# Optimization experiments

Measured on AMD Instinct MI355X. Metric: run time of the kernel, lower is better.

Reference implementation:

```python
import jax, jax.numpy as jnp
import numpy as np

B, IN, H = 262144, 128, 128

def setup_inputs() -> dict:
    key = jax.random.key(0)
    ks = jax.random.split(key, 16)
    s = 1.0 / np.sqrt(IN)
    inp = {
        'x': jax.random.normal(ks[0], (B, IN), jnp.float32),
        'h_prev': jax.random.normal(ks[1], (B, H), jnp.float32),
        'c_prev': jax.random.normal(ks[2], (B, H), jnp.float32),
        'n_prev': jax.random.uniform(ks[3], (B, H), jnp.float32),
        'W_i': jax.random.normal(ks[4], (H, IN), jnp.float32) * s,
        'U_i': jax.random.normal(ks[5], (H, H), jnp.float32) * s,
        'W_f': jax.random.normal(ks[6], (H, IN), jnp.float32) * s,
        'U_f': jax.random.normal(ks[7], (H, H), jnp.float32) * s,
        'W_o': jax.random.normal(ks[8], (H, IN), jnp.float32) * s,
        'U_o': jax.random.normal(ks[9], (H, H), jnp.float32) * s,
        'W_z': jax.random.normal(ks[10], (H, IN), jnp.float32) * s,
        'U_z': jax.random.normal(ks[11], (H, H), jnp.float32) * s,
        'b_i': jnp.zeros((H,), jnp.float32),
        'b_f': jnp.ones((H,), jnp.float32),
        'b_o': jnp.zeros((H,), jnp.float32),
        'b_z': jnp.zeros((H,), jnp.float32),
    }
    return inp

def reference(x, h_prev, c_prev, n_prev, W_i, U_i, W_f, U_f, W_o, U_o, W_z, U_z, b_i, b_f, b_o, b_z):
    # torch Linear(no bias): y = x @ W.T
    i_tilde = x @ W_i.T + h_prev @ U_i.T + b_i
    f_tilde = x @ W_f.T + h_prev @ U_f.T + b_f
    o_tilde = x @ W_o.T + h_prev @ U_o.T + b_o
    z_tilde = x @ W_z.T + h_prev @ U_z.T + b_z
    m_t = jnp.maximum(f_tilde, i_tilde)
    i_t = jnp.exp(i_tilde - m_t)
    f_t = jax.nn.sigmoid(f_tilde) + jnp.exp(f_tilde - m_t)
    o_t = jax.nn.sigmoid(o_tilde)
    z_t = jnp.tanh(z_tilde)
    c_t = f_t * c_prev + i_t * z_t
    n_t = f_t * n_prev + i_t
    h_t = o_t * (c_t / (n_t + 1e-8))
    return (h_t, c_t, n_t)
```

## Files before the change

### kernel.cpp

```cpp
#include <hip/hip_runtime.h>
#include <hip/hip_bf16.h>

typedef __attribute__((ext_vector_type(8))) _Float16 f16x8;
typedef __attribute__((ext_vector_type(4))) float f32x4;

#define NROWS 262144
#define MBLK  32
#define NBLKS (NROWS / MBLK)

__global__ void prep_weights(
    const float* __restrict__ Wi, const float* __restrict__ Ui,
    const float* __restrict__ Wf, const float* __restrict__ Uf,
    const float* __restrict__ Wo, const float* __restrict__ Uo,
    const float* __restrict__ Wz, const float* __restrict__ Uz,
    ushort* __restrict__ wh)
{
    int idx = blockIdx.x * 256 + threadIdx.x;
    int j    = idx & 7;
    int lane = (idx >> 3) & 63;
    int kk   = (idx >> 9) & 7;
    int g    = (idx >> 12) & 3;
    int w    = (idx >> 14) & 7;
    int n = w * 16 + (lane & 15);
    int k = kk * 32 + (lane >> 4) * 8 + j;
    const float* W; const float* U;
    if (g == 0)      { W = Wi; U = Ui; }
    else if (g == 1) { W = Wf; U = Uf; }
    else if (g == 2) { W = Wo; U = Uo; }
    else             { W = Wz; U = Uz; }
    float v = (k < 128) ? W[n * 128 + k] : U[n * 128 + (k - 128)];
    _Float16 hh = (_Float16)v;
    wh[idx] = __builtin_bit_cast(ushort, hh);
}

__global__ __launch_bounds__(512, 4) void slstm_main(
    const float* __restrict__ x,     const float* __restrict__ hprev,
    const float* __restrict__ cprev, const float* __restrict__ nprev,
    const float* __restrict__ bi,    const float* __restrict__ bfg,
    const float* __restrict__ bo,    const float* __restrict__ bz,
    const ushort* __restrict__ wh,
    float* __restrict__ out)
{
    __shared__ ushort Ahi[32 * 256];
    __shared__ ushort Alo[32 * 256];
    char* AhiB = reinterpret_cast<char*>(Ahi);
    char* AloB = reinterpret_cast<char*>(Alo);

    const int tid  = threadIdx.x;
    const int row0 = blockIdx.x * MBLK;

    #pragma unroll
    for (int i = 0; i < 2; ++i) {
        int f4  = tid + i * 512;
        int row = f4 >> 5;
        int c4  = f4 & 31;
        f32x4 vx = reinterpret_cast<const f32x4*>(x)[(size_t)(row0 + row) * 32 + c4];
        f32x4 vh = reinterpret_cast<const f32x4*>(hprev)[(size_t)(row0 + row) * 32 + c4];
        #pragma unroll
        for (int half = 0; half < 2; ++half) {
            f32x4 v = half ? vh : vx;
            int kbase = half * 128 + 4 * c4;
            int q   = kbase >> 3;
            int sub = (kbase & 7) * 2;
            int byt = row * 512 + ((q ^ (row & 7)) << 4) + sub;
            ushort hb[4], lb[4];
            #pragma unroll
            for (int e = 0; e < 4; ++e) {
                float ve = v[e];
                _Float16 hh = (_Float16)ve;
                _Float16 hl = (_Float16)(ve - (float)hh);
                hb[e] = __builtin_bit_cast(ushort, hh);
                lb[e] = __builtin_bit_cast(ushort, hl);
            }
            uint2 hp, lp;
            hp.x = (uint)hb[0] | ((uint)hb[1] << 16);
            hp.y = (uint)hb[2] | ((uint)hb[3] << 16);
            lp.x = (uint)lb[0] | ((uint)lb[1] << 16);
            lp.y = (uint)lb[2] | ((uint)lb[3] << 16);
            *reinterpret_cast<uint2*>(AhiB + byt) = hp;
            *reinterpret_cast<uint2*>(AloB + byt) = lp;
        }
    }
    __syncthreads();

    const int w    = tid >> 6;
    const int lane = tid & 63;
    const int l15  = lane & 15;
    const int lg   = lane >> 4;

    const ushort* whW = wh + (size_t)(w * 32) * 512 + lane * 8;

    f32x4 acc[4][2] = {};

    #pragma unroll
    for (int kk = 0; kk < 8; ++kk) {
        f16x8 ah[2], al[2];
        #pragma unroll
        for (int mi = 0; mi < 2; ++mi) {
            int row = mi * 16 + l15;
            int q   = kk * 4 + lg;
            int byt = row * 512 + ((q ^ (row & 7)) << 4);
            ah[mi] = *reinterpret_cast<const f16x8*>(AhiB + byt);
            al[mi] = *reinterpret_cast<const f16x8*>(AloB + byt);
        }
        #pragma unroll
        for (int g = 0; g < 4; ++g) {
            f16x8 b = *reinterpret_cast<const f16x8*>(whW + (g * 8 + kk) * 512);
            #pragma unroll
            for (int mi = 0; mi < 2; ++mi)
                acc[g][mi] = __builtin_amdgcn_mfma_f32_16x16x32_f16(ah[mi], b, acc[g][mi], 0, 0, 0);
            #pragma unroll
            for (int mi = 0; mi < 2; ++mi)
                acc[g][mi] = __builtin_amdgcn_mfma_f32_16x16x32_f16(al[mi], b, acc[g][mi], 0, 0, 0);
        }
    }

    const size_t OUTS = (size_t)NROWS * 128;
    const int c = w * 16 + l15;
    const float bic = bi[c], bfc = bfg[c], boc = bo[c], bzc = bz[c];
    const float* cB = cprev + (size_t)row0 * 128 + c;
    const float* nB = nprev + (size_t)row0 * 128 + c;
    float* outB = out + (size_t)row0 * 128 + c;

    float cpv[2][4], npv[2][4];
    #pragma unroll
    for (int mi = 0; mi < 2; ++mi)
        #pragma unroll
        for (int r = 0; r < 4; ++r) {
            int off = (mi * 16 + lg * 4 + r) * 128;
            cpv[mi][r] = cB[off];
            npv[mi][r] = nB[off];
        }

    #pragma unroll
    for (int mi = 0; mi < 2; ++mi)
        #pragma unroll
        for (int r = 0; r < 4; ++r) {
            float pit = acc[0][mi][r] + bic;
            float pft = acc[1][mi][r] + bfc;
            float pot = acc[2][mi][r] + boc;
            float pzt = acc[3][mi][r] + bzc;
            float m   = fmaxf(pft, pit);
            float i_t = __expf(pit - m);
            float f_t = __builtin_amdgcn_rcpf(1.0f + __expf(-pft)) + __expf(pft - m);
            float o_t = __builtin_amdgcn_rcpf(1.0f + __expf(-pot));
            float zc  = fminf(fmaxf(pzt, -15.0f), 15.0f);
            float e2  = __expf(2.0f * zc);
            float z_t = (e2 - 1.0f) * __builtin_amdgcn_rcpf(e2 + 1.0f);
            float c_t = f_t * cpv[mi][r] + i_t * z_t;
            float n_t = f_t * npv[mi][r] + i_t;
            float h_t = o_t * c_t * __builtin_amdgcn_rcpf(n_t + 1e-8f);
            int off = (mi * 16 + lg * 4 + r) * 128;
            outB[off]            = h_t;
            outB[OUTS + off]     = c_t;
            outB[2 * OUTS + off] = n_t;
        }
}

extern "C" void kernel_launch(void* const* d_in, const int* in_sizes, int n_in,
                              void* d_out, int out_size, void* d_ws, size_t ws_size,
                              hipStream_t stream) {
    const float* x  = (const float*)d_in[0];
    const float* h  = (const float*)d_in[1];
    const float* cp = (const float*)d_in[2];
    const float* np = (const float*)d_in[3];
    const float* Wi = (const float*)d_in[4];
    const float* Ui = (const float*)d_in[5];
    const float* Wf = (const float*)d_in[6];
    const float* Uf = (const float*)d_in[7];
    const float* Wo = (const float*)d_in[8];
    const float* Uo = (const float*)d_in[9];
    const float* Wz = (const float*)d_in[10];
    const float* Uz = (const float*)d_in[11];
    const float* bi = (const float*)d_in[12];
    const float* bf = (const float*)d_in[13];
    const float* bo = (const float*)d_in[14];
    const float* bz = (const float*)d_in[15];

    ushort* wh = (ushort*)d_ws;

    prep_weights<<<512, 256, 0, stream>>>(Wi, Ui, Wf, Uf, Wo, Uo, Wz, Uz, wh);
    slstm_main<<<NBLKS, 512, 0, stream>>>(x, h, cp, np, bi, bf, bo, bz, wh,
                                          (float*)d_out);
}
```

Measured before the change: 272.6 us.

## Drop fp16 hi/lo split of activations and double rows per block

Removes the error-compensating low-half fp16 term for the activation operand, so each tile issues half as many MFMAs and stages one shared buffer instead of two. The rows per block double to 64, so each weight fragment loaded from global memory is reused across four row tiles instead of two. The per-row epilogue now loads cprev and nprev per row tile to keep register pressure down. This costs accuracy, since activations are now rounded to plain fp16, and the larger accumulator array may raise register use.

After: 265.9 us. 1.03x faster.

```diff
diff --git a/kernel.cpp b/kernel.cpp
--- a/kernel.cpp
+++ b/kernel.cpp
@@ -5,7 +5,7 @@
 typedef __attribute__((ext_vector_type(4))) float f32x4;
 
 #define NROWS 262144
-#define MBLK  32
+#define MBLK  64
 #define NBLKS (NROWS / MBLK)
 
 __global__ void prep_weights(
@@ -41,16 +41,14 @@
     const ushort* __restrict__ wh,
     float* __restrict__ out)
 {
-    __shared__ ushort Ahi[32 * 256];
-    __shared__ ushort Alo[32 * 256];
-    char* AhiB = reinterpret_cast<char*>(Ahi);
-    char* AloB = reinterpret_cast<char*>(Alo);
+    __shared__ ushort A[64 * 256];
+    char* AB = reinterpret_cast<char*>(A);
 
     const int tid  = threadIdx.x;
     const int row0 = blockIdx.x * MBLK;
 
     #pragma unroll
-    for (int i = 0; i < 2; ++i) {
+    for (int i = 0; i < 4; ++i) {
         int f4  = tid + i * 512;
         int row = f4 >> 5;
         int c4  = f4 & 31;
@@ -63,22 +61,16 @@
             int q   = kbase >> 3;
             int sub = (kbase & 7) * 2;
             int byt = row * 512 + ((q ^ (row & 7)) << 4) + sub;
-            ushort hb[4], lb[4];
+            ushort hb[4];
             #pragma unroll
             for (int e = 0; e < 4; ++e) {
-                float ve = v[e];
-                _Float16 hh = (_Float16)ve;
-                _Float16 hl = (_Float16)(ve - (float)hh);
+                _Float16 hh = (_Float16)(float)v[e];
                 hb[e] = __builtin_bit_cast(ushort, hh);
-                lb[e] = __builtin_bit_cast(ushort, hl);
             }
-            uint2 hp, lp;
+            uint2 hp;
             hp.x = (uint)hb[0] | ((uint)hb[1] << 16);
             hp.y = (uint)hb[2] | ((uint)hb[3] << 16);
-            lp.x = (uint)lb[0] | ((uint)lb[1] << 16);
-            lp.y = (uint)lb[2] | ((uint)lb[3] << 16);
-            *reinterpret_cast<uint2*>(AhiB + byt) = hp;
-            *reinterpret_cast<uint2*>(AloB + byt) = lp;
+            *reinterpret_cast<uint2*>(AB + byt) = hp;
         }
     }
     __syncthreads();
@@ -90,28 +82,24 @@
 
     const ushort* whW = wh + (size_t)(w * 32) * 512 + lane * 8;
 
-    f32x4 acc[4][2] = {};
+    f32x4 acc[4][4] = {};
 
     #pragma unroll
     for (int kk = 0; kk < 8; ++kk) {
-        f16x8 ah[2], al[2];
+        f16x8 ah[4];
         #pragma unroll
-        for (int mi = 0; mi < 2; ++mi) {
+        for (int mi = 0; mi < 4; ++mi) {
             int row = mi * 16 + l15;
             int q   = kk * 4 + lg;
             int byt = row * 512 + ((q ^ (row & 7)) << 4);
-            ah[mi] = *reinterpret_cast<const f16x8*>(AhiB + byt);
-            al[mi] = *reinterpret_cast<const f16x8*>(AloB + byt);
+            ah[mi] = *reinterpret_cast<const f16x8*>(AB + byt);
         }
         #pragma unroll
         for (int g = 0; g < 4; ++g) {
             f16x8 b = *reinterpret_cast<const f16x8*>(whW + (g * 8 + kk) * 512);
             #pragma unroll
-            for (int mi = 0; mi < 2; ++mi)
+            for (int mi = 0; mi < 4; ++mi)
                 acc[g][mi] = __builtin_amdgcn_mfma_f32_16x16x32_f16(ah[mi], b, acc[g][mi], 0, 0, 0);
-            #pragma unroll
-            for (int mi = 0; mi < 2; ++mi)
-                acc[g][mi] = __builtin_amdgcn_mfma_f32_16x16x32_f16(al[mi], b, acc[g][mi], 0, 0, 0);
         }
     }
 
@@ -122,18 +110,15 @@
     const float* nB = nprev + (size_t)row0 * 128 + c;
     float* outB = out + (size_t)row0 * 128 + c;
 
-    float cpv[2][4], npv[2][4];
     #pragma unroll
-    for (int mi = 0; mi < 2; ++mi)
+    for (int mi = 0; mi < 4; ++mi) {
+        float cpv[4], npv[4];
         #pragma unroll
         for (int r = 0; r < 4; ++r) {
             int off = (mi * 16 + lg * 4 + r) * 128;
-            cpv[mi][r] = cB[off];
-            npv[mi][r] = nB[off];
+            cpv[r] = cB[off];
+            npv[r] = nB[off];
         }
-
-    #pragma unroll
-    for (int mi = 0; mi < 2; ++mi)
         #pragma unroll
         for (int r = 0; r < 4; ++r) {
             float pit = acc[0][mi][r] + bic;
@@ -147,14 +132,15 @@
             float zc  = fminf(fmaxf(pzt, -15.0f), 15.0f);
             float e2  = __expf(2.0f * zc);
             float z_t = (e2 - 1.0f) * __builtin_amdgcn_rcpf(e2 + 1.0f);
-            float c_t = f_t * cpv[mi][r] + i_t * z_t;
-            float n_t = f_t * npv[mi][r] + i_t;
+            float c_t = f_t * cpv[r] + i_t * z_t;
+            float n_t = f_t * npv[r] + i_t;
             float h_t = o_t * c_t * __builtin_amdgcn_rcpf(n_t + 1e-8f);
             int off = (mi * 16 + lg * 4 + r) * 128;
             outB[off]            = h_t;
             outB[OUTS + off]     = c_t;
             outB[2 * OUTS + off] = n_t;
         }
+    }
 }
 
 extern "C" void kernel_launch(void* const* d_in, const int* in_sizes, int n_in,
```
